# Performance work log

Hardware: AMD Instinct MI355X
Metric: run time of the kernel (lower is better)

Reference implementation:

```python
import jax, jax.numpy as jnp
import numpy as np

B, C, D, H, W = 4, 32, 64, 64, 64
RATIO = 2
K = 7  # spatial conv kernel


def setup_inputs() -> dict:
    key = jax.random.key(0)
    ks = jax.random.split(key, 7)
    x = jax.random.normal(ks[0], (B, C, D, H, W), dtype=jnp.float32)
    # ChannelAttention params (torch Linear: y = x @ W.T + b)
    fc1_w = jax.random.normal(ks[1], (2 * C * RATIO, 2 * C), dtype=jnp.float32) * 0.05
    fc1_b = jax.random.normal(ks[2], (2 * C * RATIO,), dtype=jnp.float32) * 0.05
    fc2_w = jax.random.normal(ks[3], (C, 2 * C * RATIO), dtype=jnp.float32) * 0.05
    fc2_b = jax.random.normal(ks[4], (C,), dtype=jnp.float32) * 0.05
    # SpatialAttention convs (no bias): conv1 2->4 k=7 pad 3, conv2 4->1 k=1
    conv1_w = jax.random.normal(ks[5], (2 * RATIO, 2, K, K, K), dtype=jnp.float32) * 0.05
    conv2_w = jax.random.normal(ks[6], (1, 2 * RATIO, 1, 1, 1), dtype=jnp.float32) * 0.05
    return {"x": x, "fc1_w": fc1_w, "fc1_b": fc1_b, "fc2_w": fc2_w,
            "fc2_b": fc2_b, "conv1_w": conv1_w, "conv2_w": conv2_w}


def _conv3d(x, w, padding):
    return jax.lax.conv_general_dilated(
        x, w, window_strides=(1, 1, 1), padding=padding,
        dimension_numbers=("NCDHW", "OIDHW", "NCDHW"))


def reference(x, fc1_w, fc1_b, fc2_w, fc2_b, conv1_w, conv2_w):
    # --- ChannelAttention: ca [B, C] ---
    x_avg = jnp.mean(x, axis=(2, 3, 4))  # [B, C]
    x_max = jnp.max(x, axis=(2, 3, 4))   # [B, C]
    h = jnp.concatenate([x_avg, x_max], axis=1)  # [B, 2C]
    h = jax.nn.relu(h @ fc1_w.T + fc1_b)
    ca = jax.nn.sigmoid(h @ fc2_w.T + fc2_b)     # [B, C]

    # --- SpatialAttention: sa [B, 1, D, H, W] ---
    avg_out = jnp.mean(x, axis=1, keepdims=True)
    max_out = jnp.max(x, axis=1, keepdims=True)
    s = jnp.concatenate([avg_out, max_out], axis=1)  # [B, 2, D, H, W]
    s = jax.nn.relu(_conv3d(s, conv1_w, "SAME"))     # k=7, pad=3 == SAME
    sa = jax.nn.sigmoid(_conv3d(s, conv2_w, "VALID"))  # [B, 1, D, H, W]

    # fused broadcast replacing the per-(i,j) python loop:
    # attention[b, c] = sa[b, 0] * ca[b, c]
    attention = sa * ca[:, :, None, None, None]  # [B, C, D, H, W]
    anti_attention = 1.0 - attention
    return attention, anti_attention
```

## Files before the change

kernel.cpp:

```cpp
#include <hip/hip_runtime.h>
#include <math.h>

#define Bn 4
#define Cn 32
#define Dn 64
#define Hn 64
#define Wn 64
#define HW (Hn * Wn)
#define DHW (Dn * Hn * Wn)
#define TOT (Bn * Cn * DHW)
#define NCHUNK 128

typedef float f4 __attribute__((ext_vector_type(4)));

__global__ __launch_bounds__(256) void reduce_kernel(
    const float* __restrict__ x,
    float* __restrict__ s_avg, float* __restrict__ s_max,
    float* __restrict__ part_sum, float* __restrict__ part_max) {
    const int b = blockIdx.x / NCHUNK;
    const int chunk = blockIdx.x % NCHUNK;
    const int base = chunk * 2048 + threadIdx.x * 4;
    const int lane = threadIdx.x & 63;
    const int wid = threadIdx.x >> 6;

    f4 ssum0 = {0.f, 0.f, 0.f, 0.f}, ssum1 = {0.f, 0.f, 0.f, 0.f};
    f4 smax0 = {-INFINITY, -INFINITY, -INFINITY, -INFINITY};
    f4 smax1 = smax0;
    float tsum[Cn], tmax[Cn];

    const float* xp = x + (size_t)b * Cn * DHW + base;
#pragma unroll
    for (int c = 0; c < Cn; ++c) {
        const f4 v0 = *reinterpret_cast<const f4*>(xp + (size_t)c * DHW);
        const f4 v1 = *reinterpret_cast<const f4*>(xp + (size_t)c * DHW + 1024);
        ssum0 += v0; ssum1 += v1;
        smax0.x = fmaxf(smax0.x, v0.x); smax0.y = fmaxf(smax0.y, v0.y);
        smax0.z = fmaxf(smax0.z, v0.z); smax0.w = fmaxf(smax0.w, v0.w);
        smax1.x = fmaxf(smax1.x, v1.x); smax1.y = fmaxf(smax1.y, v1.y);
        smax1.z = fmaxf(smax1.z, v1.z); smax1.w = fmaxf(smax1.w, v1.w);
        const float s0 = (v0.x + v0.y) + (v0.z + v0.w);
        const float s1 = (v1.x + v1.y) + (v1.z + v1.w);
        tsum[c] = s0 + s1;
        const float m0 = fmaxf(fmaxf(v0.x, v0.y), fmaxf(v0.z, v0.w));
        const float m1 = fmaxf(fmaxf(v1.x, v1.y), fmaxf(v1.z, v1.w));
        tmax[c] = fmaxf(m0, m1);
    }

    float* avp = s_avg + (size_t)b * DHW + base;
    float* mxp = s_max + (size_t)b * DHW + base;
    *reinterpret_cast<f4*>(avp) = ssum0 * (1.f / Cn);
    *reinterpret_cast<f4*>(avp + 1024) = ssum1 * (1.f / Cn);
    *reinterpret_cast<f4*>(mxp) = smax0;
    *reinterpret_cast<f4*>(mxp + 1024) = smax1;

    __shared__ float redS[4][Cn];
    __shared__ float redM[4][Cn];
#pragma unroll
    for (int c = 0; c < Cn; ++c) {
        float ps = tsum[c], pm = tmax[c];
#pragma unroll
        for (int off = 32; off; off >>= 1) {
            ps += __shfl_xor(ps, off);
            pm = fmaxf(pm, __shfl_xor(pm, off));
        }
        if (lane == 0) { redS[wid][c] = ps; redM[wid][c] = pm; }
    }
    __syncthreads();
    if (threadIdx.x < Cn) {
        const int c = threadIdx.x;
        float s = (redS[0][c] + redS[1][c]) + (redS[2][c] + redS[3][c]);
        float m = fmaxf(fmaxf(redM[0][c], redM[1][c]),
                        fmaxf(redM[2][c], redM[3][c]));
        part_sum[(b * Cn + c) * NCHUNK + chunk] = s;
        part_max[(b * Cn + c) * NCHUNK + chunk] = m;
    }
}

__global__ __launch_bounds__(256) void ca_kernel(
    const float* __restrict__ part_sum, const float* __restrict__ part_max,
    const float* __restrict__ fc1_w, const float* __restrict__ fc1_b,
    const float* __restrict__ fc2_w, const float* __restrict__ fc2_b,
    float* __restrict__ ca) {
    __shared__ float inpAll[Bn][64];
    __shared__ float h[128];
    const int t = threadIdx.x;
    {
        const int which = t >> 7;
        const int b = (t >> 5) & 3;
        const int c = t & 31;
        const f4* p4 = reinterpret_cast<const f4*>(
            (which ? part_max : part_sum) + (b * Cn + c) * NCHUNK);
        if (which == 0) {
            float acc = 0.f;
#pragma unroll
            for (int i = 0; i < NCHUNK / 4; ++i) {
                f4 v = p4[i];
                acc += (v.x + v.y) + (v.z + v.w);
            }
            inpAll[b][c] = acc * (1.f / DHW);
        } else {
            float m = -INFINITY;
#pragma unroll
            for (int i = 0; i < NCHUNK / 4; ++i) {
                f4 v = p4[i];
                m = fmaxf(m, fmaxf(fmaxf(v.x, v.y), fmaxf(v.z, v.w)));
            }
            inpAll[b][Cn + c] = m;
        }
    }
    __syncthreads();
#pragma unroll 1
    for (int b = 0; b < Bn; ++b) {
        if (t < 128) {
            float acc = fc1_b[t];
#pragma unroll
            for (int k = 0; k < 64; ++k) acc += fc1_w[t * 64 + k] * inpAll[b][k];
            h[t] = fmaxf(acc, 0.f);
        }
        __syncthreads();
        if (t < Cn) {
            float a2 = fc2_b[t];
#pragma unroll
            for (int k = 0; k < 128; ++k) a2 += fc2_w[t * 128 + k] * h[k];
            ca[b * Cn + t] = 1.f / (1.f + expf(-a2));
        }
        __syncthreads();
    }
}

#define TZc 4
#define TYc 4
#define LXc (Wn + 6)
#define LYc (TYc + 6)
#define LZc (TZc + 6)
#define HALO1 (LZc * LYc * LXc)

__global__ __launch_bounds__(256) void conv_kernel(
    const float* __restrict__ ca_g,
    const float* __restrict__ s_avg, const float* __restrict__ s_max,
    const float* __restrict__ w1, const float* __restrict__ w2,
    float* __restrict__ out) {
    __shared__ float sIn[HALO1];
    __shared__ float sv_s[TZc * TYc * Wn];
    __shared__ float ca_s[Cn];

    const int t = threadIdx.x;
    const int bid = blockIdx.x;
    const int b = bid >> 8;
    const int tile = bid & 255;
    const int tz = tile >> 4, ty = tile & 15;
    const int z0 = tz * TZc, y0 = ty * TYc;

    if (t < Cn) ca_s[t] = ca_g[b * Cn + t];

    const float* srcA = s_avg + (size_t)b * DHW;
    const float* srcM = s_max + (size_t)b * DHW;

    const int lx = t & 63, ly = t >> 6;

    float acc[4][TZc];
#pragma unroll
    for (int oc = 0; oc < 4; ++oc)
#pragma unroll
        for (int o = 0; o < TZc; ++o) acc[oc][o] = 0.f;

#pragma unroll 1
    for (int ic = 0; ic < 2; ++ic) {
        __syncthreads();
        const float* src = ic ? srcM : srcA;
        for (int i = t; i < HALO1; i += 256) {
            const int xx = i % LXc;
            const int rem = i / LXc;
            const int yy = rem % LYc;
            const int zz = rem / LYc;
            const int gz = z0 + zz - 3, gy = y0 + yy - 3, gx = xx - 3;
            float v = 0.f;
            if ((unsigned)gz < (unsigned)Dn && (unsigned)gy < (unsigned)Hn &&
                (unsigned)gx < (unsigned)Wn)
                v = src[(gz * Hn + gy) * Wn + gx];
            sIn[i] = v;
        }
        __syncthreads();

#pragma unroll 1
        for (int kh = 0; kh < 7; ++kh)
#pragma unroll 1
            for (int kw = 0; kw < 7; ++kw) {
                float incol[LZc];
#pragma unroll
                for (int s = 0; s < LZc; ++s)
                    incol[s] = sIn[(s * LYc + (ly + kh)) * LXc + (lx + kw)];
#pragma unroll
                for (int kd = 0; kd < 7; ++kd)
#pragma unroll
                    for (int oc = 0; oc < 4; ++oc) {
                        float w = w1[(((oc * 2 + ic) * 7 + kd) * 7 + kh) * 7 + kw];
#pragma unroll
                        for (int o = 0; o < TZc; ++o)
                            acc[oc][o] += incol[o + kd] * w;
                    }
            }
    }

    const float c20 = w2[0], c21 = w2[1], c22 = w2[2], c23 = w2[3];
#pragma unroll
    for (int o = 0; o < TZc; ++o) {
        float s = fmaxf(acc[0][o], 0.f) * c20 + fmaxf(acc[1][o], 0.f) * c21 +
                  fmaxf(acc[2][o], 0.f) * c22 + fmaxf(acc[3][o], 0.f) * c23;
        sv_s[(o * TYc + ly) * Wn + lx] = 1.f / (1.f + expf(-s));
    }
    __syncthreads();

    const int wv = t >> 6, ln = t & 63;
    const f4* sv4 = reinterpret_cast<const f4*>(sv_s);
    f4* out4 = reinterpret_cast<f4*>(out);
    const size_t totq4 = TOT / 4;
#pragma unroll 1
    for (int combo = wv; combo < Cn * TZc; combo += 4) {
        const int c = combo >> 2, oz = combo & 3;
        const float cav = ca_s[c];
        const f4 v = sv4[oz * 64 + ln];
        const f4 att = v * cav;
        const f4 anti = 1.f - att;
        const size_t off = (((size_t)(b * Cn + c) * DHW) >> 2) +
                           (size_t)(z0 + oz) * (HW / 4) +
                           (size_t)y0 * (Wn / 4) + ln;
        __builtin_nontemporal_store(att, &out4[off]);
        __builtin_nontemporal_store(anti, &out4[totq4 + off]);
    }
}

extern "C" void kernel_launch(void* const* d_in, const int* in_sizes, int n_in,
                              void* d_out, int out_size, void* d_ws,
                              size_t ws_size, hipStream_t stream) {
    const float* x = (const float*)d_in[0];
    const float* fc1_w = (const float*)d_in[1];
    const float* fc1_b = (const float*)d_in[2];
    const float* fc2_w = (const float*)d_in[3];
    const float* fc2_b = (const float*)d_in[4];
    const float* conv1_w = (const float*)d_in[5];
    const float* conv2_w = (const float*)d_in[6];

    float* ws = (float*)d_ws;
    float* s_avg = ws;
    float* s_max = s_avg + (size_t)Bn * DHW;
    float* part_sum = s_max + (size_t)Bn * DHW;
    float* part_max = part_sum + Bn * Cn * NCHUNK;
    float* ca = part_max + Bn * Cn * NCHUNK;

    reduce_kernel<<<Bn * NCHUNK, 256, 0, stream>>>(x, s_avg, s_max, part_sum,
                                                   part_max);
    ca_kernel<<<1, 256, 0, stream>>>(part_sum, part_max, fc1_w, fc1_b, fc2_w,
                                     fc2_b, ca);
    conv_kernel<<<Bn * 256, 256, 0, stream>>>(ca, s_avg, s_max, conv1_w,
                                              conv2_w, (float*)d_out);
}
```

Measured before the change: 159.3 us.

## Halve conv tile height, use 128-thread blocks, write outputs directly from registers

Shrinks the conv tile from 4 to 2 rows in y, giving twice as many blocks of 128 threads. Each thread now stores its own per-voxel results straight to global memory as scalar nontemporal stores, dropping the shared-memory staging buffer and its barrier. The accumulators are split into four separate arrays with the four output-channel weights hoisted per kd. The aim is more parallelism and less synchronization, at the cost of larger relative halo overhead (8 vs 10 rows loaded per 2 vs 4 output rows) and narrower scalar stores in place of 16-byte vector stores.

Measured after the change: 219.9 us. 38.0% more time.

```diff
diff --git a/kernel.cpp b/kernel.cpp
--- a/kernel.cpp
+++ b/kernel.cpp
@@ -129,26 +129,25 @@
 }
 
 #define TZc 4
-#define TYc 4
+#define TYc 2
 #define LXc (Wn + 6)
 #define LYc (TYc + 6)
 #define LZc (TZc + 6)
 #define HALO1 (LZc * LYc * LXc)
 
-__global__ __launch_bounds__(256) void conv_kernel(
+__global__ __launch_bounds__(128) void conv_kernel(
     const float* __restrict__ ca_g,
     const float* __restrict__ s_avg, const float* __restrict__ s_max,
     const float* __restrict__ w1, const float* __restrict__ w2,
     float* __restrict__ out) {
     __shared__ float sIn[HALO1];
-    __shared__ float sv_s[TZc * TYc * Wn];
     __shared__ float ca_s[Cn];
 
     const int t = threadIdx.x;
     const int bid = blockIdx.x;
-    const int b = bid >> 8;
-    const int tile = bid & 255;
-    const int tz = tile >> 4, ty = tile & 15;
+    const int b = bid >> 9;
+    const int tile = bid & 511;
+    const int tz = tile >> 5, ty = tile & 31;
     const int z0 = tz * TZc, y0 = ty * TYc;
 
     if (t < Cn) ca_s[t] = ca_g[b * Cn + t];
@@ -158,17 +157,16 @@
 
     const int lx = t & 63, ly = t >> 6;
 
-    float acc[4][TZc];
-#pragma unroll
-    for (int oc = 0; oc < 4; ++oc)
-#pragma unroll
-        for (int o = 0; o < TZc; ++o) acc[oc][o] = 0.f;
+    float a0[TZc] = {0.f, 0.f, 0.f, 0.f};
+    float a1[TZc] = {0.f, 0.f, 0.f, 0.f};
+    float a2[TZc] = {0.f, 0.f, 0.f, 0.f};
+    float a3[TZc] = {0.f, 0.f, 0.f, 0.f};
 
 #pragma unroll 1
     for (int ic = 0; ic < 2; ++ic) {
         __syncthreads();
         const float* src = ic ? srcM : srcA;
-        for (int i = t; i < HALO1; i += 256) {
+        for (int i = t; i < HALO1; i += 128) {
             const int xx = i % LXc;
             const int rem = i / LXc;
             const int yy = rem % LYc;
@@ -189,44 +187,47 @@
                 float incol[LZc];
 #pragma unroll
                 for (int s = 0; s < LZc; ++s)
-                    incol[s] = sIn[(s * LYc + (ly + kh)) * LXc + (lx + kw)];
-#pragma unroll
-                for (int kd = 0; kd < 7; ++kd)
-#pragma unroll
-                    for (int oc = 0; oc < 4; ++oc) {
-                        float w = w1[(((oc * 2 + ic) * 7 + kd) * 7 + kh) * 7 + kw];
-#pragma unroll
-                        for (int o = 0; o < TZc; ++o)
-                            acc[oc][o] += incol[o + kd] * w;
+                    incol[s] =
+                        sIn[(s * LYc + (ly + kh)) * LXc + (lx + kw)];
+#pragma unroll
+                for (int kd = 0; kd < 7; ++kd) {
+                    const float w0 = w1[((0 * 2 + ic) * 343) + kd * 49 + kh * 7 + kw];
+                    const float w1v = w1[((1 * 2 + ic) * 343) + kd * 49 + kh * 7 + kw];
+                    const float w2v = w1[((2 * 2 + ic) * 343) + kd * 49 + kh * 7 + kw];
+                    const float w3v = w1[((3 * 2 + ic) * 343) + kd * 49 + kh * 7 + kw];
+#pragma unroll
+                    for (int o = 0; o < TZc; ++o) {
+                        const float iv = incol[o + kd];
+                        a0[o] += iv * w0;
+                        a1[o] += iv * w1v;
+                        a2[o] += iv * w2v;
+                        a3[o] += iv * w3v;
                     }
+                }
             }
     }
 
     const float c20 = w2[0], c21 = w2[1], c22 = w2[2], c23 = w2[3];
+    float sv[TZc];
 #pragma unroll
     for (int o = 0; o < TZc; ++o) {
-        float s = fmaxf(acc[0][o], 0.f) * c20 + fmaxf(acc[1][o], 0.f) * c21 +
-                  fmaxf(acc[2][o], 0.f) * c22 + fmaxf(acc[3][o], 0.f) * c23;
-        sv_s[(o * TYc + ly) * Wn + lx] = 1.f / (1.f + expf(-s));
-    }
-    __syncthreads();
-
-    const int wv = t >> 6, ln = t & 63;
-    const f4* sv4 = reinterpret_cast<const f4*>(sv_s);
-    f4* out4 = reinterpret_cast<f4*>(out);
-    const size_t totq4 = TOT / 4;
-#pragma unroll 1
-    for (int combo = wv; combo < Cn * TZc; combo += 4) {
-        const int c = combo >> 2, oz = combo & 3;
+        float s = fmaxf(a0[o], 0.f) * c20 + fmaxf(a1[o], 0.f) * c21 +
+                  fmaxf(a2[o], 0.f) * c22 + fmaxf(a3[o], 0.f) * c23;
+        sv[o] = 1.f / (1.f + expf(-s));
+    }
+
+    const size_t base = (size_t)b * Cn * DHW + (size_t)z0 * HW +
+                        (size_t)(y0 + ly) * Wn + lx;
+#pragma unroll 1
+    for (int c = 0; c < Cn; ++c) {
         const float cav = ca_s[c];
-        const f4 v = sv4[oz * 64 + ln];
-        const f4 att = v * cav;
-        const f4 anti = 1.f - att;
-        const size_t off = (((size_t)(b * Cn + c) * DHW) >> 2) +
-                           (size_t)(z0 + oz) * (HW / 4) +
-                           (size_t)y0 * (Wn / 4) + ln;
-        __builtin_nontemporal_store(att, &out4[off]);
-        __builtin_nontemporal_store(anti, &out4[totq4 + off]);
+        const size_t cb = base + (size_t)c * DHW;
+#pragma unroll
+        for (int o = 0; o < TZc; ++o) {
+            const float a = sv[o] * cav;
+            __builtin_nontemporal_store(a, out + cb + o * HW);
+            __builtin_nontemporal_store(1.f - a, out + TOT + cb + o * HW);
+        }
     }
 }
 
@@ -252,6 +253,6 @@
                                                    part_max);
     ca_kernel<<<1, 256, 0, stream>>>(part_sum, part_max, fc1_w, fc1_b, fc2_w,
                                      fc2_b, ca);
-    conv_kernel<<<Bn * 256, 256, 0, stream>>>(ca, s_avg, s_max, conv1_w,
+    conv_kernel<<<Bn * 512, 128, 0, stream>>>(ca, s_avg, s_max, conv1_w,
                                               conv2_w, (float*)d_out);
 }
```
